# Optimization experiments

Hardware: AMD Instinct MI355X
Metric: run time of the kernel (lower is better)

Reference implementation:

```python
import jax, jax.numpy as jnp
import numpy as np

FOUR_PI = 4.0 * 3.14159265358979323846


def winding_numbers(points, tris):
    """Generalized winding number of `points` w.r.t. triangle soup `tris`.
    points: [B, P, 3]; tris: [B, F, 3, 3]. Returns [B, P].
    Uses the van Oosterom-Strackee solid-angle formula per triangle.
    """
    # relative vectors from each point to each triangle vertex: [B, P, F, 3, 3]
    r = tris[:, None, :, :, :] - points[:, :, None, None, :]
    a, b, c = r[..., 0, :], r[..., 1, :], r[..., 2, :]
    la = jnp.linalg.norm(a, axis=-1)
    lb = jnp.linalg.norm(b, axis=-1)
    lc = jnp.linalg.norm(c, axis=-1)
    det = jnp.sum(a * jnp.cross(b, c), axis=-1)
    denom = (la * lb * lc
             + jnp.sum(a * b, axis=-1) * lc
             + jnp.sum(b * c, axis=-1) * la
             + jnp.sum(c * a, axis=-1) * lb)
    omega = 2.0 * jnp.arctan2(det, denom)  # signed solid angle per triangle
    return jnp.sum(omega, axis=-1) / FOUR_PI  # [B, P]


def setup_inputs() -> dict:
    key = jax.random.key(0)
    k1, k2, k3, k4, k5 = jax.random.split(key, 5)
    B, V, Vs, F, LB = 4, 6890, 1024, 2048, 64
    vertices = jax.random.normal(k1, (B, V, 3), dtype=jnp.float32)
    segment_vidx = jax.random.randint(k2, (Vs,), 0, V).astype(jnp.int64)
    band0_idx = jax.random.randint(k3, (LB,), 0, V).astype(jnp.int64)
    band1_idx = jax.random.randint(k4, (LB,), 0, V).astype(jnp.int64)
    # closed mesh has V + 2 vertices (one appended mean vertex per band)
    segment_faces = jax.random.randint(k5, (F, 3), 0, V + 2).astype(jnp.int64)
    return {"vertices": vertices, "segment_vidx": segment_vidx,
            "band0_idx": band0_idx, "band1_idx": band1_idx,
            "segment_faces": segment_faces}


def reference(vertices, segment_vidx, band0_idx, band1_idx, segment_faces):
    # get_closed_segment: append the mean vertex of each boundary band
    b0 = jnp.mean(vertices[:, band0_idx, :], axis=1, keepdims=True)  # [B,1,3]
    b1 = jnp.mean(vertices[:, band1_idx, :], axis=1, keepdims=True)  # [B,1,3]
    segm_verts = jnp.concatenate([vertices, b0, b1], axis=1)         # [B,V+2,3]
    segm_triangles = segm_verts[:, segment_faces]                    # [B,F,3,3]
    pts = vertices[:, segment_vidx, :]                               # [B,Vs,3]
    wn = winding_numbers(pts, segm_triangles)                        # [B,Vs]
    # original: exterior = wn <= 0.99 (boolean); we return the float winding
    # numbers as the kernel-relevant output; threshold is a trivial epilogue.
    return wn
```

## Files before the change

### kernel.cpp

```cpp
#include <hip/hip_runtime.h>
#include <math.h>

#define INV_TWO_PI 0.15915494309189535f
#define PPB 4

__device__ __forceinline__ float fast_atan2f(float y, float x) {
    const float PI   = 3.14159265358979f;
    const float PI_2 = 1.57079632679490f;
    float ax = fabsf(x), ay = fabsf(y);
    float mx = fmaxf(ax, ay), mn = fminf(ax, ay);
    float inv = __builtin_amdgcn_rcpf(mx);
    float t = (mx > 0.f) ? mn * inv : 0.f;
    float s = t * t;
    float r = -0.0040540580f;
    r = fmaf(r, s, 0.0218612288f);
    r = fmaf(r, s, -0.0559098861f);
    r = fmaf(r, s, 0.0964200441f);
    r = fmaf(r, s, -0.1390853351f);
    r = fmaf(r, s, 0.1994653599f);
    r = fmaf(r, s, -0.3332985605f);
    r = fmaf(r, s, 0.9999993329f);
    r = r * t;
    if (ay > ax) r = PI_2 - r;
    if (x < 0.f) r = PI - r;
    return copysignf(r, y);
}

__device__ __forceinline__ float solid_angle_atan(
    float v0x, float v0y, float v0z,
    float v1x, float v1y, float v1z,
    float v2x, float v2y, float v2z,
    float px, float py, float pz) {
    float ax = v0x - px, ay = v0y - py, az = v0z - pz;
    float bx = v1x - px, by = v1y - py, bz = v1z - pz;
    float cx = v2x - px, cy = v2y - py, cz = v2z - pz;

    float la = __builtin_amdgcn_sqrtf(fmaf(ax, ax, fmaf(ay, ay, az * az)));
    float lb = __builtin_amdgcn_sqrtf(fmaf(bx, bx, fmaf(by, by, bz * bz)));
    float lc = __builtin_amdgcn_sqrtf(fmaf(cx, cx, fmaf(cy, cy, cz * cz)));

    float crx = by * cz - bz * cy;
    float cry = bz * cx - bx * cz;
    float crz = bx * cy - by * cx;
    float det = ax * crx + ay * cry + az * crz;

    float dab = fmaf(ax, bx, fmaf(ay, by, az * bz));
    float dbc = fmaf(bx, cx, fmaf(by, cy, bz * cz));
    float dca = fmaf(cx, ax, fmaf(cy, ay, cz * az));
    float den = fmaf(la * lb, lc, fmaf(dab, lc, fmaf(dbc, la, dca * lb)));

    return fast_atan2f(det, den);
}

__global__ void band_means_kernel(const float* __restrict__ verts,
                                  const int* __restrict__ b0i,
                                  const int* __restrict__ b1i,
                                  float* __restrict__ bands,
                                  int V, int LB) {
    int b = blockIdx.x;
    int t = threadIdx.x;
    float s[6] = {0.f, 0.f, 0.f, 0.f, 0.f, 0.f};
    for (int i = t; i < LB; i += 64) {
        int i0 = b0i[i];
        int i1 = b1i[i];
        const float* p0 = verts + ((size_t)b * V + i0) * 3;
        const float* p1 = verts + ((size_t)b * V + i1) * 3;
        s[0] += p0[0]; s[1] += p0[1]; s[2] += p0[2];
        s[3] += p1[0]; s[4] += p1[1]; s[5] += p1[2];
    }
#pragma unroll
    for (int off = 32; off; off >>= 1) {
#pragma unroll
        for (int c = 0; c < 6; ++c) s[c] += __shfl_down(s[c], off, 64);
    }
    if (t == 0) {
        float inv = 1.0f / (float)LB;
#pragma unroll
        for (int c = 0; c < 6; ++c) bands[b * 6 + c] = s[c] * inv;
    }
}

__global__ void gather_tris_kernel(const float* __restrict__ verts,
                                   const int* __restrict__ faces,
                                   const float* __restrict__ bands,
                                   float* __restrict__ tri,
                                   int B, int V, int F) {
    int idx = blockIdx.x * blockDim.x + threadIdx.x;
    if (idx >= B * F) return;
    int f = idx % F;
    int b = idx / F;
    float v[3][3];
#pragma unroll
    for (int k = 0; k < 3; ++k) {
        int vi = faces[f * 3 + k];
        const float* s = (vi < V) ? (verts + ((size_t)b * V + vi) * 3)
                                  : (bands + b * 6 + (size_t)(vi - V) * 3);
        v[k][0] = s[0]; v[k][1] = s[1]; v[k][2] = s[2];
    }
    float4* d = (float4*)(tri + (size_t)idx * 12);
    d[0] = make_float4(v[0][0], v[0][1], v[0][2], v[1][0]);
    d[1] = make_float4(v[1][1], v[1][2], v[2][0], v[2][1]);
    d[2] = make_float4(v[2][2], 0.f, 0.f, 0.f);
}

__global__ __launch_bounds__(256) void winding4_kernel(
    const float* __restrict__ tri,
    const float* __restrict__ verts,
    const int* __restrict__ vidx,
    float* __restrict__ out,
    int P, int F, int V) {
    int nPB = (P + PPB - 1) / PPB;
    int b  = blockIdx.x / nPB;
    int pb = blockIdx.x - b * nPB;
    int p0 = pb * PPB;
    int tid = threadIdx.x;

    float px[PPB], py[PPB], pz[PPB], acc[PPB];
#pragma unroll
    for (int j = 0; j < PPB; ++j) {
        int p = (p0 + j < P) ? (p0 + j) : (P - 1);
        const float* pt = verts + ((size_t)b * V + vidx[p]) * 3;
        px[j] = pt[0]; py[j] = pt[1]; pz[j] = pt[2];
        acc[j] = 0.f;
    }

    const float4* tb = (const float4*)(tri + (size_t)b * F * 12);
    for (int f = tid; f < F; f += 256) {
        float4 q0 = tb[(size_t)f * 3 + 0];
        float4 q1 = tb[(size_t)f * 3 + 1];
        float4 q2 = tb[(size_t)f * 3 + 2];
#pragma unroll
        for (int j = 0; j < PPB; ++j) {
            acc[j] += solid_angle_atan(q0.x, q0.y, q0.z,
                                       q0.w, q1.x, q1.y,
                                       q1.z, q1.w, q2.x,
                                       px[j], py[j], pz[j]);
        }
    }

#pragma unroll
    for (int off = 32; off; off >>= 1) {
#pragma unroll
        for (int j = 0; j < PPB; ++j) acc[j] += __shfl_down(acc[j], off, 64);
    }

    __shared__ float part[4][PPB];
    int wid = tid >> 6;
    if ((tid & 63) == 0) {
#pragma unroll
        for (int j = 0; j < PPB; ++j) part[wid][j] = acc[j];
    }
    __syncthreads();
    if (tid < PPB) {
        int p = p0 + tid;
        if (p < P) {
            float tot = part[0][tid] + part[1][tid] + part[2][tid] + part[3][tid];
            out[(size_t)b * P + p] = tot * INV_TWO_PI;
        }
    }
}

__global__ __launch_bounds__(256) void winding_fallback_kernel(
    const float* __restrict__ verts,
    const int* __restrict__ vidx,
    const int* __restrict__ faces,
    const float* __restrict__ bands,
    float* __restrict__ out,
    int P, int F, int V) {
    int blk = blockIdx.x;
    int b = blk / P;
    int p = blk - b * P;
    int tid = threadIdx.x;

    const float* pt = verts + ((size_t)b * V + vidx[p]) * 3;
    float px = pt[0], py = pt[1], pz = pt[2];
    float b0x = bands[b * 6 + 0], b0y = bands[b * 6 + 1], b0z = bands[b * 6 + 2];
    float b1x = bands[b * 6 + 3], b1y = bands[b * 6 + 4], b1z = bands[b * 6 + 5];

    float acc = 0.f;
    for (int f = tid; f < F; f += 256) {
        float vv[3][3];
#pragma unroll
        for (int k = 0; k < 3; ++k) {
            int vi = faces[f * 3 + k];
            if (vi < V) {
                const float* s = verts + ((size_t)b * V + vi) * 3;
                vv[k][0] = s[0]; vv[k][1] = s[1]; vv[k][2] = s[2];
            } else if (vi == V) {
                vv[k][0] = b0x; vv[k][1] = b0y; vv[k][2] = b0z;
            } else {
                vv[k][0] = b1x; vv[k][1] = b1y; vv[k][2] = b1z;
            }
        }
        acc += solid_angle_atan(vv[0][0], vv[0][1], vv[0][2],
                                vv[1][0], vv[1][1], vv[1][2],
                                vv[2][0], vv[2][1], vv[2][2],
                                px, py, pz);
    }
#pragma unroll
    for (int off = 32; off; off >>= 1) acc += __shfl_down(acc, off, 64);
    __shared__ float part[4];
    int wid = tid >> 6;
    if ((tid & 63) == 0) part[wid] = acc;
    __syncthreads();
    if (tid == 0) {
        out[(size_t)b * P + p] = (part[0] + part[1] + part[2] + part[3]) * INV_TWO_PI;
    }
}

extern "C" void kernel_launch(void* const* d_in, const int* in_sizes, int n_in,
                              void* d_out, int out_size, void* d_ws, size_t ws_size,
                              hipStream_t stream) {
    const float* verts = (const float*)d_in[0];
    const int* svidx   = (const int*)d_in[1];
    const int* b0i     = (const int*)d_in[2];
    const int* b1i     = (const int*)d_in[3];
    const int* faces   = (const int*)d_in[4];
    float* out = (float*)d_out;

    int P  = in_sizes[1];
    int LB = in_sizes[2];
    int F  = in_sizes[4] / 3;
    int B  = out_size / P;
    int V  = in_sizes[0] / (3 * B);

    float* bands = (float*)d_ws;
    size_t tri_off = 256;
    size_t tri_bytes = (size_t)B * F * 12 * sizeof(float);
    bool use_prep = (ws_size >= tri_off + tri_bytes);
    float* tri = (float*)((char*)d_ws + tri_off);

    band_means_kernel<<<B, 64, 0, stream>>>(verts, b0i, b1i, bands, V, LB);

    if (use_prep) {
        int tot = B * F;
        gather_tris_kernel<<<(tot + 255) / 256, 256, 0, stream>>>(verts, faces, bands, tri, B, V, F);
        int nPB = (P + PPB - 1) / PPB;
        winding4_kernel<<<B * nPB, 256, 0, stream>>>(tri, verts, svidx, out, P, F, V);
    } else {
        winding_fallback_kernel<<<B * P, 256, 0, stream>>>(verts, svidx, faces, bands, out, P, F, V);
    }
}
```

Measured before the change: 83.12 us.

## Swap work decomposition: threads own points, blocks own face chunks, separate reduce

Each thread now holds four query points and loops over a small chunk of faces (eight per block), reading the face data as uniform broadcast loads. Per-chunk partial sums go to a workspace buffer and a separate kernel reduces them. This removes the cross-lane shuffle reduction and the per-thread strided triangle loads. The band-mean computation is folded into the gather kernel, and triangles are padded to 16 floats. The cost is a large partial buffer (NF*B*P floats), one extra launch for the reduction, and more global write traffic.

```diff
diff --git a/kernel.cpp b/kernel.cpp
--- a/kernel.cpp
+++ b/kernel.cpp
@@ -3,6 +3,7 @@
 
 #define INV_TWO_PI 0.15915494309189535f
 #define PPB 4
+#define FPB 8
 
 __device__ __forceinline__ float fast_atan2f(float y, float x) {
     const float PI   = 3.14159265358979f;
@@ -52,6 +53,125 @@
     return fast_atan2f(det, den);
 }
 
+__global__ void gather_tris_kernel(const float* __restrict__ verts,
+                                   const int* __restrict__ b0i,
+                                   const int* __restrict__ b1i,
+                                   const int* __restrict__ faces,
+                                   float* __restrict__ tri,
+                                   int B, int V, int F, int LB, int nfc) {
+    int b  = blockIdx.x / nfc;
+    int fc = blockIdx.x - b * nfc;
+    int tid = threadIdx.x;
+    int wid = tid >> 6, lane = tid & 63;
+
+    __shared__ float sband[6];
+    if (wid < 2) {
+        const int* bi = wid ? b1i : b0i;
+        float sx = 0.f, sy = 0.f, sz = 0.f;
+        for (int i = lane; i < LB; i += 64) {
+            int vi = bi[i];
+            const float* q = verts + ((size_t)b * V + vi) * 3;
+            sx += q[0]; sy += q[1]; sz += q[2];
+        }
+#pragma unroll
+        for (int off = 32; off; off >>= 1) {
+            sx += __shfl_down(sx, off, 64);
+            sy += __shfl_down(sy, off, 64);
+            sz += __shfl_down(sz, off, 64);
+        }
+        if (lane == 0) {
+            float inv = 1.0f / (float)LB;
+            sband[wid * 3 + 0] = sx * inv;
+            sband[wid * 3 + 1] = sy * inv;
+            sband[wid * 3 + 2] = sz * inv;
+        }
+    }
+    __syncthreads();
+
+    int f = fc * 256 + tid;
+    if (f >= F) return;
+    float v[3][3];
+#pragma unroll
+    for (int k = 0; k < 3; ++k) {
+        int vi = faces[f * 3 + k];
+        if (vi < V) {
+            const float* s = verts + ((size_t)b * V + vi) * 3;
+            v[k][0] = s[0]; v[k][1] = s[1]; v[k][2] = s[2];
+        } else {
+            int j = (vi - V) * 3;
+            v[k][0] = sband[j + 0]; v[k][1] = sband[j + 1]; v[k][2] = sband[j + 2];
+        }
+    }
+    float4* d = (float4*)(tri + ((size_t)b * F + f) * 16);
+    d[0] = make_float4(v[0][0], v[0][1], v[0][2], v[1][0]);
+    d[1] = make_float4(v[1][1], v[1][2], v[2][0], v[2][1]);
+    d[2] = make_float4(v[2][2], 0.f, 0.f, 0.f);
+    d[3] = make_float4(0.f, 0.f, 0.f, 0.f);
+}
+
+__global__ __launch_bounds__(256) void winding_bcast_kernel(
+    const float* __restrict__ tri,
+    const float* __restrict__ verts,
+    const int* __restrict__ vidx,
+    float* __restrict__ partial,
+    int P, int F, int V, int B, int NF) {
+    int b = blockIdx.x / NF;
+    int s = blockIdx.x - b * NF;
+    int f0 = s * FPB;
+    int tid = threadIdx.x;
+
+    float px[PPB], py[PPB], pz[PPB], acc[PPB];
+#pragma unroll
+    for (int j = 0; j < PPB; ++j) {
+        int p = j * 256 + tid;
+        int pc = (p < P) ? p : (P - 1);
+        const float* pt = verts + ((size_t)b * V + vidx[pc]) * 3;
+        px[j] = pt[0]; py[j] = pt[1]; pz[j] = pt[2];
+        acc[j] = 0.f;
+    }
+
+    const float* tb = tri + (size_t)b * F * 16;
+#pragma unroll
+    for (int i = 0; i < FPB; ++i) {
+        int f = f0 + i;
+        if (f < F) {
+            const float* r = tb + (size_t)f * 16;
+            float v0x = r[0], v0y = r[1], v0z = r[2];
+            float v1x = r[3], v1y = r[4], v1z = r[5];
+            float v2x = r[6], v2y = r[7], v2z = r[8];
+#pragma unroll
+            for (int j = 0; j < PPB; ++j) {
+                acc[j] += solid_angle_atan(v0x, v0y, v0z, v1x, v1y, v1z,
+                                           v2x, v2y, v2z, px[j], py[j], pz[j]);
+            }
+        }
+    }
+
+    float* dst = partial + ((size_t)s * B + b) * P;
+#pragma unroll
+    for (int j = 0; j < PPB; ++j) {
+        int p = j * 256 + tid;
+        if (p < P) dst[p] = acc[j];
+    }
+}
+
+__global__ void reduce_kernel(const float* __restrict__ partial,
+                              float* __restrict__ out, int BP, int NF) {
+    int idx = blockIdx.x * blockDim.x + threadIdx.x;
+    if (idx >= BP) return;
+    const float* p = partial + idx;
+    float a0 = 0.f, a1 = 0.f, a2 = 0.f, a3 = 0.f;
+    int s = 0;
+    for (; s + 4 <= NF; s += 4) {
+        a0 += p[(size_t)(s + 0) * BP];
+        a1 += p[(size_t)(s + 1) * BP];
+        a2 += p[(size_t)(s + 2) * BP];
+        a3 += p[(size_t)(s + 3) * BP];
+    }
+    for (; s < NF; ++s) a0 += p[(size_t)s * BP];
+    out[idx] = ((a0 + a1) + (a2 + a3)) * INV_TWO_PI;
+}
+
 __global__ void band_means_kernel(const float* __restrict__ verts,
                                   const int* __restrict__ b0i,
                                   const int* __restrict__ b1i,
@@ -80,86 +200,6 @@
     }
 }
 
-__global__ void gather_tris_kernel(const float* __restrict__ verts,
-                                   const int* __restrict__ faces,
-                                   const float* __restrict__ bands,
-                                   float* __restrict__ tri,
-                                   int B, int V, int F) {
-    int idx = blockIdx.x * blockDim.x + threadIdx.x;
-    if (idx >= B * F) return;
-    int f = idx % F;
-    int b = idx / F;
-    float v[3][3];
-#pragma unroll
-    for (int k = 0; k < 3; ++k) {
-        int vi = faces[f * 3 + k];
-        const float* s = (vi < V) ? (verts + ((size_t)b * V + vi) * 3)
-                                  : (bands + b * 6 + (size_t)(vi - V) * 3);
-        v[k][0] = s[0]; v[k][1] = s[1]; v[k][2] = s[2];
-    }
-    float4* d = (float4*)(tri + (size_t)idx * 12);
-    d[0] = make_float4(v[0][0], v[0][1], v[0][2], v[1][0]);
-    d[1] = make_float4(v[1][1], v[1][2], v[2][0], v[2][1]);
-    d[2] = make_float4(v[2][2], 0.f, 0.f, 0.f);
-}
-
-__global__ __launch_bounds__(256) void winding4_kernel(
-    const float* __restrict__ tri,
-    const float* __restrict__ verts,
-    const int* __restrict__ vidx,
-    float* __restrict__ out,
-    int P, int F, int V) {
-    int nPB = (P + PPB - 1) / PPB;
-    int b  = blockIdx.x / nPB;
-    int pb = blockIdx.x - b * nPB;
-    int p0 = pb * PPB;
-    int tid = threadIdx.x;
-
-    float px[PPB], py[PPB], pz[PPB], acc[PPB];
-#pragma unroll
-    for (int j = 0; j < PPB; ++j) {
-        int p = (p0 + j < P) ? (p0 + j) : (P - 1);
-        const float* pt = verts + ((size_t)b * V + vidx[p]) * 3;
-        px[j] = pt[0]; py[j] = pt[1]; pz[j] = pt[2];
-        acc[j] = 0.f;
-    }
-
-    const float4* tb = (const float4*)(tri + (size_t)b * F * 12);
-    for (int f = tid; f < F; f += 256) {
-        float4 q0 = tb[(size_t)f * 3 + 0];
-        float4 q1 = tb[(size_t)f * 3 + 1];
-        float4 q2 = tb[(size_t)f * 3 + 2];
-#pragma unroll
-        for (int j = 0; j < PPB; ++j) {
-            acc[j] += solid_angle_atan(q0.x, q0.y, q0.z,
-                                       q0.w, q1.x, q1.y,
-                                       q1.z, q1.w, q2.x,
-                                       px[j], py[j], pz[j]);
-        }
-    }
-
-#pragma unroll
-    for (int off = 32; off; off >>= 1) {
-#pragma unroll
-        for (int j = 0; j < PPB; ++j) acc[j] += __shfl_down(acc[j], off, 64);
-    }
-
-    __shared__ float part[4][PPB];
-    int wid = tid >> 6;
-    if ((tid & 63) == 0) {
-#pragma unroll
-        for (int j = 0; j < PPB; ++j) part[wid][j] = acc[j];
-    }
-    __syncthreads();
-    if (tid < PPB) {
-        int p = p0 + tid;
-        if (p < P) {
-            float tot = part[0][tid] + part[1][tid] + part[2][tid] + part[3][tid];
-            out[(size_t)b * P + p] = tot * INV_TWO_PI;
-        }
-    }
-}
-
 __global__ __launch_bounds__(256) void winding_fallback_kernel(
     const float* __restrict__ verts,
     const int* __restrict__ vidx,
@@ -224,20 +264,28 @@
     int B  = out_size / P;
     int V  = in_sizes[0] / (3 * B);
 
-    float* bands = (float*)d_ws;
-    size_t tri_off = 256;
-    size_t tri_bytes = (size_t)B * F * 12 * sizeof(float);
-    bool use_prep = (ws_size >= tri_off + tri_bytes);
-    float* tri = (float*)((char*)d_ws + tri_off);
-
-    band_means_kernel<<<B, 64, 0, stream>>>(verts, b0i, b1i, bands, V, LB);
-
-    if (use_prep) {
-        int tot = B * F;
-        gather_tris_kernel<<<(tot + 255) / 256, 256, 0, stream>>>(verts, faces, bands, tri, B, V, F);
-        int nPB = (P + PPB - 1) / PPB;
-        winding4_kernel<<<B * nPB, 256, 0, stream>>>(tri, verts, svidx, out, P, F, V);
+    int NF = (F + FPB - 1) / FPB;
+    int pts_per_block = 256 * PPB;
+
+    size_t tri_bytes  = (size_t)B * F * 16 * sizeof(float);
+    size_t tri_pad    = (tri_bytes + 255) & ~(size_t)255;
+    size_t part_bytes = (size_t)NF * B * P * sizeof(float);
+    bool use_bcast = (P <= pts_per_block) && (ws_size >= tri_pad + part_bytes);
+
+    if (use_bcast) {
+        float* tri     = (float*)d_ws;
+        float* partial = (float*)((char*)d_ws + tri_pad);
+        int nfc = (F + 255) / 256;
+        gather_tris_kernel<<<B * nfc, 256, 0, stream>>>(verts, b0i, b1i, faces,
+                                                        tri, B, V, F, LB, nfc);
+        winding_bcast_kernel<<<B * NF, 256, 0, stream>>>(tri, verts, svidx,
+                                                         partial, P, F, V, B, NF);
+        int BP = B * P;
+        reduce_kernel<<<(BP + 255) / 256, 256, 0, stream>>>(partial, out, BP, NF);
     } else {
-        winding_fallback_kernel<<<B * P, 256, 0, stream>>>(verts, svidx, faces, bands, out, P, F, V);
-    }
-}
+        float* bands = (float*)d_ws;
+        band_means_kernel<<<B, 64, 0, stream>>>(verts, b0i, b1i, bands, V, LB);
+        winding_fallback_kernel<<<B * P, 256, 0, stream>>>(verts, svidx, faces,
+                                                           bands, out, P, F, V);
+    }
+}
```

Measured after the change: 101.6 us. +22.2%, slower.

## Fuse band-mean computation into triangle gather and prefetch next triangle in winding loop

Applied to the files above, without the earlier changes.

The separate band-mean kernel is folded into the triangle-gather kernel. Each block recomputes both band means into shared memory before gathering its faces, which removes one launch and its dependency. The winding kernel now software-pipelines its triangle loads, fetching the next face's data while computing the current one. The cost is redundant band-mean work in every gather block and extra registers for the prefetched triangle.

```diff
diff --git a/kernel.cpp b/kernel.cpp
--- a/kernel.cpp
+++ b/kernel.cpp
@@ -52,6 +52,133 @@
     return fast_atan2f(det, den);
 }
 
+__global__ void gather_tris_kernel(const float* __restrict__ verts,
+                                   const int* __restrict__ b0i,
+                                   const int* __restrict__ b1i,
+                                   const int* __restrict__ faces,
+                                   float* __restrict__ tri,
+                                   int B, int V, int F, int LB, int nfc) {
+    int b  = blockIdx.x / nfc;
+    int fc = blockIdx.x - b * nfc;
+    int tid = threadIdx.x;
+    int wid = tid >> 6, lane = tid & 63;
+
+    __shared__ float sband[6];
+    if (wid < 2) {
+        const int* bi = wid ? b1i : b0i;
+        float sx = 0.f, sy = 0.f, sz = 0.f;
+        for (int i = lane; i < LB; i += 64) {
+            int vi = bi[i];
+            const float* q = verts + ((size_t)b * V + vi) * 3;
+            sx += q[0]; sy += q[1]; sz += q[2];
+        }
+#pragma unroll
+        for (int off = 32; off; off >>= 1) {
+            sx += __shfl_down(sx, off, 64);
+            sy += __shfl_down(sy, off, 64);
+            sz += __shfl_down(sz, off, 64);
+        }
+        if (lane == 0) {
+            float inv = 1.0f / (float)LB;
+            sband[wid * 3 + 0] = sx * inv;
+            sband[wid * 3 + 1] = sy * inv;
+            sband[wid * 3 + 2] = sz * inv;
+        }
+    }
+    __syncthreads();
+
+    int f = fc * 256 + tid;
+    if (f >= F) return;
+    float v[3][3];
+#pragma unroll
+    for (int k = 0; k < 3; ++k) {
+        int vi = faces[f * 3 + k];
+        if (vi < V) {
+            const float* s = verts + ((size_t)b * V + vi) * 3;
+            v[k][0] = s[0]; v[k][1] = s[1]; v[k][2] = s[2];
+        } else {
+            int j = (vi - V) * 3;
+            v[k][0] = sband[j + 0]; v[k][1] = sband[j + 1]; v[k][2] = sband[j + 2];
+        }
+    }
+    float4* d = (float4*)(tri + ((size_t)b * F + f) * 12);
+    d[0] = make_float4(v[0][0], v[0][1], v[0][2], v[1][0]);
+    d[1] = make_float4(v[1][1], v[1][2], v[2][0], v[2][1]);
+    d[2] = make_float4(v[2][2], 0.f, 0.f, 0.f);
+}
+
+__global__ __launch_bounds__(256) void winding4_kernel(
+    const float* __restrict__ tri,
+    const float* __restrict__ verts,
+    const int* __restrict__ vidx,
+    float* __restrict__ out,
+    int P, int F, int V) {
+    int nPB = (P + PPB - 1) / PPB;
+    int b  = blockIdx.x / nPB;
+    int pb = blockIdx.x - b * nPB;
+    int p0 = pb * PPB;
+    int tid = threadIdx.x;
+
+    const float4* tb = (const float4*)(tri + (size_t)b * F * 12);
+
+    int f = tid;
+    float4 q0 = make_float4(0.f, 0.f, 0.f, 0.f), q1 = q0, q2 = q0;
+    if (f < F) {
+        q0 = tb[(size_t)f * 3 + 0];
+        q1 = tb[(size_t)f * 3 + 1];
+        q2 = tb[(size_t)f * 3 + 2];
+    }
+
+    float px[PPB], py[PPB], pz[PPB], acc[PPB];
+#pragma unroll
+    for (int j = 0; j < PPB; ++j) {
+        int p = (p0 + j < P) ? (p0 + j) : (P - 1);
+        const float* pt = verts + ((size_t)b * V + vidx[p]) * 3;
+        px[j] = pt[0]; py[j] = pt[1]; pz[j] = pt[2];
+        acc[j] = 0.f;
+    }
+
+    while (f < F) {
+        int fn = f + 256;
+        float4 n0 = q0, n1 = q1, n2 = q2;
+        if (fn < F) {
+            n0 = tb[(size_t)fn * 3 + 0];
+            n1 = tb[(size_t)fn * 3 + 1];
+            n2 = tb[(size_t)fn * 3 + 2];
+        }
+#pragma unroll
+        for (int j = 0; j < PPB; ++j) {
+            acc[j] += solid_angle_atan(q0.x, q0.y, q0.z,
+                                       q0.w, q1.x, q1.y,
+                                       q1.z, q1.w, q2.x,
+                                       px[j], py[j], pz[j]);
+        }
+        q0 = n0; q1 = n1; q2 = n2;
+        f = fn;
+    }
+
+#pragma unroll
+    for (int off = 32; off; off >>= 1) {
+#pragma unroll
+        for (int j = 0; j < PPB; ++j) acc[j] += __shfl_down(acc[j], off, 64);
+    }
+
+    __shared__ float part[4][PPB];
+    int wid = tid >> 6;
+    if ((tid & 63) == 0) {
+#pragma unroll
+        for (int j = 0; j < PPB; ++j) part[wid][j] = acc[j];
+    }
+    __syncthreads();
+    if (tid < PPB) {
+        int p = p0 + tid;
+        if (p < P) {
+            float tot = part[0][tid] + part[1][tid] + part[2][tid] + part[3][tid];
+            out[(size_t)b * P + p] = tot * INV_TWO_PI;
+        }
+    }
+}
+
 __global__ void band_means_kernel(const float* __restrict__ verts,
                                   const int* __restrict__ b0i,
                                   const int* __restrict__ b1i,
@@ -80,86 +207,6 @@
     }
 }
 
-__global__ void gather_tris_kernel(const float* __restrict__ verts,
-                                   const int* __restrict__ faces,
-                                   const float* __restrict__ bands,
-                                   float* __restrict__ tri,
-                                   int B, int V, int F) {
-    int idx = blockIdx.x * blockDim.x + threadIdx.x;
-    if (idx >= B * F) return;
-    int f = idx % F;
-    int b = idx / F;
-    float v[3][3];
-#pragma unroll
-    for (int k = 0; k < 3; ++k) {
-        int vi = faces[f * 3 + k];
-        const float* s = (vi < V) ? (verts + ((size_t)b * V + vi) * 3)
-                                  : (bands + b * 6 + (size_t)(vi - V) * 3);
-        v[k][0] = s[0]; v[k][1] = s[1]; v[k][2] = s[2];
-    }
-    float4* d = (float4*)(tri + (size_t)idx * 12);
-    d[0] = make_float4(v[0][0], v[0][1], v[0][2], v[1][0]);
-    d[1] = make_float4(v[1][1], v[1][2], v[2][0], v[2][1]);
-    d[2] = make_float4(v[2][2], 0.f, 0.f, 0.f);
-}
-
-__global__ __launch_bounds__(256) void winding4_kernel(
-    const float* __restrict__ tri,
-    const float* __restrict__ verts,
-    const int* __restrict__ vidx,
-    float* __restrict__ out,
-    int P, int F, int V) {
-    int nPB = (P + PPB - 1) / PPB;
-    int b  = blockIdx.x / nPB;
-    int pb = blockIdx.x - b * nPB;
-    int p0 = pb * PPB;
-    int tid = threadIdx.x;
-
-    float px[PPB], py[PPB], pz[PPB], acc[PPB];
-#pragma unroll
-    for (int j = 0; j < PPB; ++j) {
-        int p = (p0 + j < P) ? (p0 + j) : (P - 1);
-        const float* pt = verts + ((size_t)b * V + vidx[p]) * 3;
-        px[j] = pt[0]; py[j] = pt[1]; pz[j] = pt[2];
-        acc[j] = 0.f;
-    }
-
-    const float4* tb = (const float4*)(tri + (size_t)b * F * 12);
-    for (int f = tid; f < F; f += 256) {
-        float4 q0 = tb[(size_t)f * 3 + 0];
-        float4 q1 = tb[(size_t)f * 3 + 1];
-        float4 q2 = tb[(size_t)f * 3 + 2];
-#pragma unroll
-        for (int j = 0; j < PPB; ++j) {
-            acc[j] += solid_angle_atan(q0.x, q0.y, q0.z,
-                                       q0.w, q1.x, q1.y,
-                                       q1.z, q1.w, q2.x,
-                                       px[j], py[j], pz[j]);
-        }
-    }
-
-#pragma unroll
-    for (int off = 32; off; off >>= 1) {
-#pragma unroll
-        for (int j = 0; j < PPB; ++j) acc[j] += __shfl_down(acc[j], off, 64);
-    }
-
-    __shared__ float part[4][PPB];
-    int wid = tid >> 6;
-    if ((tid & 63) == 0) {
-#pragma unroll
-        for (int j = 0; j < PPB; ++j) part[wid][j] = acc[j];
-    }
-    __syncthreads();
-    if (tid < PPB) {
-        int p = p0 + tid;
-        if (p < P) {
-            float tot = part[0][tid] + part[1][tid] + part[2][tid] + part[3][tid];
-            out[(size_t)b * P + p] = tot * INV_TWO_PI;
-        }
-    }
-}
-
 __global__ __launch_bounds__(256) void winding_fallback_kernel(
     const float* __restrict__ verts,
     const int* __restrict__ vidx,
@@ -224,20 +271,20 @@
     int B  = out_size / P;
     int V  = in_sizes[0] / (3 * B);
 
-    float* bands = (float*)d_ws;
-    size_t tri_off = 256;
     size_t tri_bytes = (size_t)B * F * 12 * sizeof(float);
-    bool use_prep = (ws_size >= tri_off + tri_bytes);
-    float* tri = (float*)((char*)d_ws + tri_off);
-
-    band_means_kernel<<<B, 64, 0, stream>>>(verts, b0i, b1i, bands, V, LB);
+    bool use_prep = (ws_size >= tri_bytes);
 
     if (use_prep) {
-        int tot = B * F;
-        gather_tris_kernel<<<(tot + 255) / 256, 256, 0, stream>>>(verts, faces, bands, tri, B, V, F);
+        float* tri = (float*)d_ws;
+        int nfc = (F + 255) / 256;
+        gather_tris_kernel<<<B * nfc, 256, 0, stream>>>(verts, b0i, b1i, faces,
+                                                        tri, B, V, F, LB, nfc);
         int nPB = (P + PPB - 1) / PPB;
         winding4_kernel<<<B * nPB, 256, 0, stream>>>(tri, verts, svidx, out, P, F, V);
     } else {
-        winding_fallback_kernel<<<B * P, 256, 0, stream>>>(verts, svidx, faces, bands, out, P, F, V);
-    }
-}
+        float* bands = (float*)d_ws;
+        band_means_kernel<<<B, 64, 0, stream>>>(verts, b0i, b1i, bands, V, LB);
+        winding_fallback_kernel<<<B * P, 256, 0, stream>>>(verts, svidx, faces,
+                                                           bands, out, P, F, V);
+    }
+}
```

Result: no change. 82.38 us (-0.9%).

## Fuse band means and triangle gather into a single winding kernel

Applied to the files above, without the earlier changes.

Replaces the three-kernel pipeline (band means, triangle gather into workspace, winding) with one kernel. Each block recomputes the two band means in shared memory and gathers triangle vertices straight from the vertex array via face indices. This removes two launches and the round trip through the workspace buffer. In exchange every block redoes the band-mean reduction and issues scattered, uncoalesced vertex loads with branches, where it previously read packed float4 triangles.

```diff
diff --git a/kernel.cpp b/kernel.cpp
--- a/kernel.cpp
+++ b/kernel.cpp
@@ -52,68 +52,48 @@
     return fast_atan2f(det, den);
 }
 
-__global__ void band_means_kernel(const float* __restrict__ verts,
-                                  const int* __restrict__ b0i,
-                                  const int* __restrict__ b1i,
-                                  float* __restrict__ bands,
-                                  int V, int LB) {
-    int b = blockIdx.x;
-    int t = threadIdx.x;
-    float s[6] = {0.f, 0.f, 0.f, 0.f, 0.f, 0.f};
-    for (int i = t; i < LB; i += 64) {
-        int i0 = b0i[i];
-        int i1 = b1i[i];
-        const float* p0 = verts + ((size_t)b * V + i0) * 3;
-        const float* p1 = verts + ((size_t)b * V + i1) * 3;
-        s[0] += p0[0]; s[1] += p0[1]; s[2] += p0[2];
-        s[3] += p1[0]; s[4] += p1[1]; s[5] += p1[2];
-    }
-#pragma unroll
-    for (int off = 32; off; off >>= 1) {
-#pragma unroll
-        for (int c = 0; c < 6; ++c) s[c] += __shfl_down(s[c], off, 64);
-    }
-    if (t == 0) {
-        float inv = 1.0f / (float)LB;
-#pragma unroll
-        for (int c = 0; c < 6; ++c) bands[b * 6 + c] = s[c] * inv;
-    }
-}
-
-__global__ void gather_tris_kernel(const float* __restrict__ verts,
-                                   const int* __restrict__ faces,
-                                   const float* __restrict__ bands,
-                                   float* __restrict__ tri,
-                                   int B, int V, int F) {
-    int idx = blockIdx.x * blockDim.x + threadIdx.x;
-    if (idx >= B * F) return;
-    int f = idx % F;
-    int b = idx / F;
-    float v[3][3];
-#pragma unroll
-    for (int k = 0; k < 3; ++k) {
-        int vi = faces[f * 3 + k];
-        const float* s = (vi < V) ? (verts + ((size_t)b * V + vi) * 3)
-                                  : (bands + b * 6 + (size_t)(vi - V) * 3);
-        v[k][0] = s[0]; v[k][1] = s[1]; v[k][2] = s[2];
-    }
-    float4* d = (float4*)(tri + (size_t)idx * 12);
-    d[0] = make_float4(v[0][0], v[0][1], v[0][2], v[1][0]);
-    d[1] = make_float4(v[1][1], v[1][2], v[2][0], v[2][1]);
-    d[2] = make_float4(v[2][2], 0.f, 0.f, 0.f);
-}
-
-__global__ __launch_bounds__(256) void winding4_kernel(
-    const float* __restrict__ tri,
+__global__ __launch_bounds__(256) void winding_fused_kernel(
     const float* __restrict__ verts,
     const int* __restrict__ vidx,
+    const int* __restrict__ b0i,
+    const int* __restrict__ b1i,
+    const int* __restrict__ faces,
     float* __restrict__ out,
-    int P, int F, int V) {
+    int P, int F, int V, int LB) {
     int nPB = (P + PPB - 1) / PPB;
     int b  = blockIdx.x / nPB;
     int pb = blockIdx.x - b * nPB;
     int p0 = pb * PPB;
     int tid = threadIdx.x;
+    int wid = tid >> 6, lane = tid & 63;
+
+    __shared__ float sband[6];
+    if (wid < 2) {
+        const int* bi = wid ? b1i : b0i;
+        float sx = 0.f, sy = 0.f, sz = 0.f;
+        for (int i = lane; i < LB; i += 64) {
+            int vi = bi[i];
+            const float* q = verts + ((size_t)b * V + vi) * 3;
+            sx += q[0]; sy += q[1]; sz += q[2];
+        }
+#pragma unroll
+        for (int off = 32; off; off >>= 1) {
+            sx += __shfl_down(sx, off, 64);
+            sy += __shfl_down(sy, off, 64);
+            sz += __shfl_down(sz, off, 64);
+        }
+        if (lane == 0) {
+            float inv = 1.0f / (float)LB;
+            sband[wid * 3 + 0] = sx * inv;
+            sband[wid * 3 + 1] = sy * inv;
+            sband[wid * 3 + 2] = sz * inv;
+        }
+    }
+    __syncthreads();
+
+    float bnd[6];
+#pragma unroll
+    for (int c = 0; c < 6; ++c) bnd[c] = sband[c];
 
     float px[PPB], py[PPB], pz[PPB], acc[PPB];
 #pragma unroll
@@ -124,17 +104,23 @@
         acc[j] = 0.f;
     }
 
-    const float4* tb = (const float4*)(tri + (size_t)b * F * 12);
+    const float* vb = verts + (size_t)b * V * 3;
     for (int f = tid; f < F; f += 256) {
-        float4 q0 = tb[(size_t)f * 3 + 0];
-        float4 q1 = tb[(size_t)f * 3 + 1];
-        float4 q2 = tb[(size_t)f * 3 + 2];
+        int i0 = faces[f * 3 + 0];
+        int i1 = faces[f * 3 + 1];
+        int i2 = faces[f * 3 + 2];
+        float v0x, v0y, v0z, v1x, v1y, v1z, v2x, v2y, v2z;
+        if (i0 < V) { const float* s = vb + (size_t)i0 * 3; v0x = s[0]; v0y = s[1]; v0z = s[2]; }
+        else { int j = (i0 - V) * 3; v0x = bnd[j]; v0y = bnd[j + 1]; v0z = bnd[j + 2]; }
+        if (i1 < V) { const float* s = vb + (size_t)i1 * 3; v1x = s[0]; v1y = s[1]; v1z = s[2]; }
+        else { int j = (i1 - V) * 3; v1x = bnd[j]; v1y = bnd[j + 1]; v1z = bnd[j + 2]; }
+        if (i2 < V) { const float* s = vb + (size_t)i2 * 3; v2x = s[0]; v2y = s[1]; v2z = s[2]; }
+        else { int j = (i2 - V) * 3; v2x = bnd[j]; v2y = bnd[j + 1]; v2z = bnd[j + 2]; }
+
 #pragma unroll
         for (int j = 0; j < PPB; ++j) {
-            acc[j] += solid_angle_atan(q0.x, q0.y, q0.z,
-                                       q0.w, q1.x, q1.y,
-                                       q1.z, q1.w, q2.x,
-                                       px[j], py[j], pz[j]);
+            acc[j] += solid_angle_atan(v0x, v0y, v0z, v1x, v1y, v1z,
+                                       v2x, v2y, v2z, px[j], py[j], pz[j]);
         }
     }
 
@@ -145,7 +131,6 @@
     }
 
     __shared__ float part[4][PPB];
-    int wid = tid >> 6;
     if ((tid & 63) == 0) {
 #pragma unroll
         for (int j = 0; j < PPB; ++j) part[wid][j] = acc[j];
@@ -157,54 +142,6 @@
             float tot = part[0][tid] + part[1][tid] + part[2][tid] + part[3][tid];
             out[(size_t)b * P + p] = tot * INV_TWO_PI;
         }
-    }
-}
-
-__global__ __launch_bounds__(256) void winding_fallback_kernel(
-    const float* __restrict__ verts,
-    const int* __restrict__ vidx,
-    const int* __restrict__ faces,
-    const float* __restrict__ bands,
-    float* __restrict__ out,
-    int P, int F, int V) {
-    int blk = blockIdx.x;
-    int b = blk / P;
-    int p = blk - b * P;
-    int tid = threadIdx.x;
-
-    const float* pt = verts + ((size_t)b * V + vidx[p]) * 3;
-    float px = pt[0], py = pt[1], pz = pt[2];
-    float b0x = bands[b * 6 + 0], b0y = bands[b * 6 + 1], b0z = bands[b * 6 + 2];
-    float b1x = bands[b * 6 + 3], b1y = bands[b * 6 + 4], b1z = bands[b * 6 + 5];
-
-    float acc = 0.f;
-    for (int f = tid; f < F; f += 256) {
-        float vv[3][3];
-#pragma unroll
-        for (int k = 0; k < 3; ++k) {
-            int vi = faces[f * 3 + k];
-            if (vi < V) {
-                const float* s = verts + ((size_t)b * V + vi) * 3;
-                vv[k][0] = s[0]; vv[k][1] = s[1]; vv[k][2] = s[2];
-            } else if (vi == V) {
-                vv[k][0] = b0x; vv[k][1] = b0y; vv[k][2] = b0z;
-            } else {
-                vv[k][0] = b1x; vv[k][1] = b1y; vv[k][2] = b1z;
-            }
-        }
-        acc += solid_angle_atan(vv[0][0], vv[0][1], vv[0][2],
-                                vv[1][0], vv[1][1], vv[1][2],
-                                vv[2][0], vv[2][1], vv[2][2],
-                                px, py, pz);
-    }
-#pragma unroll
-    for (int off = 32; off; off >>= 1) acc += __shfl_down(acc, off, 64);
-    __shared__ float part[4];
-    int wid = tid >> 6;
-    if ((tid & 63) == 0) part[wid] = acc;
-    __syncthreads();
-    if (tid == 0) {
-        out[(size_t)b * P + p] = (part[0] + part[1] + part[2] + part[3]) * INV_TWO_PI;
     }
 }
 
@@ -224,20 +161,8 @@
     int B  = out_size / P;
     int V  = in_sizes[0] / (3 * B);
 
-    float* bands = (float*)d_ws;
-    size_t tri_off = 256;
-    size_t tri_bytes = (size_t)B * F * 12 * sizeof(float);
-    bool use_prep = (ws_size >= tri_off + tri_bytes);
-    float* tri = (float*)((char*)d_ws + tri_off);
-
-    band_means_kernel<<<B, 64, 0, stream>>>(verts, b0i, b1i, bands, V, LB);
-
-    if (use_prep) {
-        int tot = B * F;
-        gather_tris_kernel<<<(tot + 255) / 256, 256, 0, stream>>>(verts, faces, bands, tri, B, V, F);
-        int nPB = (P + PPB - 1) / PPB;
-        winding4_kernel<<<B * nPB, 256, 0, stream>>>(tri, verts, svidx, out, P, F, V);
-    } else {
-        winding_fallback_kernel<<<B * P, 256, 0, stream>>>(verts, svidx, faces, bands, out, P, F, V);
-    }
+    int nPB = (P + PPB - 1) / PPB;
+    winding_fused_kernel<<<B * nPB, 256, 0, stream>>>(verts, svidx, b0i, b1i,
+                                                      faces, out, P, F, V, LB);
+    (void)d_ws; (void)ws_size; (void)n_in;
 }
```

After: 88.42 us. +6.4%, slower.
